# Performance work log

Measured on AMD Instinct MI355X. Metric: run time of the kernel, lower is better.

Reference implementation:

```python
import jax, jax.numpy as jnp
import numpy as np
import math

B, H, S, D = 2, 16, 2048, 128

def setup_inputs() -> dict:
    key = jax.random.key(0)
    kq, kk, kv = jax.random.split(key, 3)
    return {
        "query": jax.random.normal(kq, (B, H, S, D), dtype=jnp.float32),
        "key": jax.random.normal(kk, (B, H, S, D), dtype=jnp.float32),
        "value": jax.random.normal(kv, (B, H, S, D), dtype=jnp.float32),
        "m": 0,  # falsy mask: original's masked_fill was non-in-place (no-op) anyway
    }

def reference(query, key, value, m):
    d = query.shape[-1]
    # scores: [B, H, S, S]
    scores = jnp.einsum("bhqd,bhkd->bhqk", query, key) / math.sqrt(d)
    # NOTE: original torch code's masked_fill is not in-place, so the mask
    # never affects scores; we faithfully skip it (m is falsy here regardless).
    p_attn = jax.nn.softmax(scores, axis=-1)
    p_val = jnp.einsum("bhqk,bhkd->bhqd", p_attn, value)
    return (p_val, p_attn)
```

## Files before the change

kernel.cpp:

```cpp
#include <hip/hip_runtime.h>
#include <hip/hip_bf16.h>
#include <math.h>

#define S_LEN 2048
#define DHEAD 128
#define NH    32
#define BM    128
#define KT    32
#define NKT   (S_LEN / KT)
#define SCALE 0.08838834764831845f
#define CMAX  16.0f

typedef __attribute__((ext_vector_type(4))) float f32x4;
typedef __attribute__((ext_vector_type(8))) _Float16 f16x8;
typedef __attribute__((ext_vector_type(8))) unsigned short u16x8;

static __device__ __forceinline__ f16x8 as_h8(u16x8 x) {
  return __builtin_bit_cast(f16x8, x);
}
static __device__ __forceinline__ unsigned short h16(float x) {
  _Float16 h = (_Float16)x;
  return __builtin_bit_cast(unsigned short, h);
}
static __device__ __forceinline__ void gl16(const void* g, void* l) {
  __builtin_amdgcn_global_load_lds(
      (const __attribute__((address_space(1))) void*)g,
      (__attribute__((address_space(3))) void*)l, 16, 0, 0);
}

__global__ __launch_bounds__(512) void attn_kernel(
    const float* __restrict__ Qg, const float* __restrict__ Kg,
    const float* __restrict__ Vg, float* __restrict__ out) {
  __shared__ __align__(16) float khf32[2][KT * DHEAD];
  __shared__ __align__(16) unsigned short vtr[2][DHEAD * KT];

  const int tid = threadIdx.x;
  const int w  = tid >> 6;
  const int l  = tid & 63;
  const int lr = l & 15;
  const int lg = l >> 4;

  const int d_  = blockIdx.x;
  const int xcd = d_ & 7;
  const int slot = d_ >> 3;
  const int bh = xcd + 8 * (slot >> 4);
  const int qb = slot & 15;

  const size_t head_off = (size_t)bh * S_LEN * DHEAD;
  const float* Qh = Qg + head_off;
  const float* Kh = Kg + head_off;
  const float* Vh = Vg + head_off;
  float* Ov = out + head_off;
  float* Pa = out + (size_t)NH * S_LEN * DHEAD + (size_t)bh * S_LEN * S_LEN;

  const int n0 = w * 128 + l;
  const int r0 = n0 >> 5, gc0 = (n0 & 31) ^ (r0 & 7);
  const int n1 = n0 + 64;
  const int r1 = n1 >> 5, gc1 = (n1 & 31) ^ (r1 & 7);
  const int gk0 = r0 * 128 + gc0 * 4;
  const int gk1 = r1 * 128 + gc1 * 4;
  float* lds_k0a = &khf32[0][(w * 128) * 4];
  float* lds_k0b = &khf32[0][(w * 128 + 64) * 4];
  float* lds_k1a = &khf32[1][(w * 128) * 4];
  float* lds_k1b = &khf32[1][(w * 128 + 64) * 4];

  auto issue_k = [&](int t, int b) {
    const float* src = Kh + (size_t)t * KT * DHEAD;
    gl16(src + gk0, b ? lds_k1a : lds_k0a);
    gl16(src + gk1, b ? lds_k1b : lds_k0b);
  };

  const int vi0 = tid, vi1 = 512 + tid;
  const int vkv0 = (vi0 >> 2) & 31, vd40 = (vi0 & 3) | ((vi0 >> 7) << 2);
  const int vkv1 = (vi1 >> 2) & 31, vd41 = (vi1 & 3) | ((vi1 >> 7) << 2);
  float4 vx0, vx1;
  auto load_v = [&](int t) {
    const float4* sv = (const float4*)(Vh + (size_t)t * KT * DHEAD);
    vx0 = sv[vkv0 * 32 + vd40];
    vx1 = sv[vkv1 * 32 + vd41];
  };
  auto write_v = [&](int b) {
    unsigned short* dst = vtr[b];
    float f0[4] = {vx0.x, vx0.y, vx0.z, vx0.w};
    float f1[4] = {vx1.x, vx1.y, vx1.z, vx1.w};
#pragma unroll
    for (int j = 0; j < 4; ++j) {
      int da = vd40 * 4 + j, db = vd41 * 4 + j;
      dst[da * 32 + (vkv0 ^ (((da >> 1) & 3) << 3))] = h16(f0[j]);
      dst[db * 32 + (vkv1 ^ (((db >> 1) & 3) << 3))] = h16(f1[j]);
    }
  };

  auto ldk = [&](int b, int row, int cc) -> f16x8 {
    const int m = row & 7;
    const float* base = b ? &khf32[1][row * 128] : &khf32[0][row * 128];
    f32x4 a = *(const f32x4*)&base[(cc ^ m) << 2];
    f32x4 c = *(const f32x4*)&base[((cc + 1) ^ m) << 2];
    f16x8 r;
    r[0] = (_Float16)a[0]; r[1] = (_Float16)a[1];
    r[2] = (_Float16)a[2]; r[3] = (_Float16)a[3];
    r[4] = (_Float16)c[0]; r[5] = (_Float16)c[1];
    r[6] = (_Float16)c[2]; r[7] = (_Float16)c[3];
    return r;
  };

  issue_k(0, 0);
  const int qrow = qb * BM + w * 16 + lr;
  const float* qptr = Qh + (size_t)qrow * DHEAD;
  f16x8 qh[4];
#pragma unroll
  for (int kc = 0; kc < 4; ++kc) {
    const float4* qp4 = (const float4*)(qptr + kc * 32 + lg * 8);
    float4 a = qp4[0], b = qp4[1];
    float xs[8] = {a.x, a.y, a.z, a.w, b.x, b.y, b.z, b.w};
#pragma unroll
    for (int i = 0; i < 8; ++i) qh[kc][i] = (_Float16)(xs[i] * SCALE);
  }

  const f32x4 zero4 = {0.f, 0.f, 0.f, 0.f};

  float esum = 0.f;
  for (int t = 0; t < NKT; ++t) {
    const int b = t & 1;
    asm volatile("s_waitcnt vmcnt(0)" ::: "memory");
    __syncthreads();
    if (t + 1 < NKT) issue_k(t + 1, b ^ 1);

    f32x4 sacc0 = zero4, sacc1 = zero4;
    __builtin_amdgcn_s_setprio(1);
#pragma unroll
    for (int kc = 0; kc < 4; ++kc) {
      const int cc = kc * 8 + lg * 2;
      f16x8 ka = ldk(b, lr, cc);
      f16x8 kb = ldk(b, lr + 16, cc);
      sacc0 = __builtin_amdgcn_mfma_f32_16x16x32_f16(ka, qh[kc], sacc0, 0, 0, 0);
      sacc1 = __builtin_amdgcn_mfma_f32_16x16x32_f16(kb, qh[kc], sacc1, 0, 0, 0);
    }
    __builtin_amdgcn_s_setprio(0);
#pragma unroll
    for (int r = 0; r < 4; ++r)
      esum += __expf(sacc0[r] - CMAX) + __expf(sacc1[r] - CMAX);
  }
  issue_k(0, 0);
  load_v(0);
  esum += __shfl_xor(esum, 16);
  esum += __shfl_xor(esum, 32);
  const float off_ = CMAX + logf(esum);

  f32x4 oacc[8];
#pragma unroll
  for (int dt = 0; dt < 8; ++dt) oacc[dt] = zero4;

  float* Prow = Pa + (size_t)(qb * BM + w * 16 + lr) * S_LEN;

  for (int t = 0; t < NKT; ++t) {
    const int b = t & 1;
    write_v(b);
    asm volatile("s_waitcnt vmcnt(0)" ::: "memory");
    __syncthreads();
    if (t + 1 < NKT) {
      issue_k(t + 1, b ^ 1);
      load_v(t + 1);
    }

    f32x4 sacc0 = zero4, sacc1 = zero4;
    __builtin_amdgcn_s_setprio(1);
#pragma unroll
    for (int kc = 0; kc < 4; ++kc) {
      const int cc = kc * 8 + lg * 2;
      f16x8 ka = ldk(b, lr, cc);
      f16x8 kb = ldk(b, lr + 16, cc);
      sacc0 = __builtin_amdgcn_mfma_f32_16x16x32_f16(ka, qh[kc], sacc0, 0, 0, 0);
      sacc1 = __builtin_amdgcn_mfma_f32_16x16x32_f16(kb, qh[kc], sacc1, 0, 0, 0);
    }
    __builtin_amdgcn_s_setprio(0);

    f32x4 pv0, pv1;
#pragma unroll
    for (int r = 0; r < 4; ++r) {
      pv0[r] = __expf(sacc0[r] - off_);
      pv1[r] = __expf(sacc1[r] - off_);
    }
    *(f32x4*)&Prow[t * KT + lg * 4] = pv0;
    *(f32x4*)&Prow[t * KT + 16 + lg * 4] = pv1;

    u16x8 pf;
    {
      unsigned pk[4];
#pragma unroll
      for (int r = 0; r < 4; ++r)
        pk[r] = __builtin_bit_cast(unsigned,
                  __builtin_amdgcn_cvt_pkrtz(pv0[r], pv1[r]));
      const int la = ((lg & 1) * 2) * 16 + lr;
      const int lb = la + 16;
      const bool hi = (lg & 2) != 0;
#pragma unroll
      for (int r = 0; r < 4; ++r) {
        unsigned ta = (unsigned)__shfl((int)pk[r], la, 64);
        unsigned tb = (unsigned)__shfl((int)pk[r], lb, 64);
        pf[r]     = (unsigned short)(hi ? (ta >> 16) : (ta & 0xffffu));
        pf[r + 4] = (unsigned short)(hi ? (tb >> 16) : (tb & 0xffffu));
      }
    }

    __builtin_amdgcn_s_setprio(1);
#pragma unroll
    for (int dt = 0; dt < 8; ++dt) {
      const int row = dt * 16 + lr;
      const unsigned short* vsrc = vtr[b];
      u16x8 vf = *(const u16x8*)&vsrc[row * 32 +
                                      ((lg * 8) ^ (((row >> 1) & 3) << 3))];
      oacc[dt] = __builtin_amdgcn_mfma_f32_16x16x32_f16(
          as_h8(pf), as_h8(vf), oacc[dt], 0, 0, 0);
    }
    __builtin_amdgcn_s_setprio(0);
  }

#pragma unroll
  for (int dt = 0; dt < 8; ++dt) {
#pragma unroll
    for (int r = 0; r < 4; ++r) {
      const int qloc = w * 16 + lg * 4 + r;
      Ov[(size_t)(qb * BM + qloc) * DHEAD + dt * 16 + lr] = oacc[dt][r];
    }
  }
}

extern "C" void kernel_launch(void* const* d_in, const int* in_sizes, int n_in,
                              void* d_out, int out_size, void* d_ws,
                              size_t ws_size, hipStream_t stream) {
  const float* Q = (const float*)d_in[0];
  const float* K = (const float*)d_in[1];
  const float* V = (const float*)d_in[2];
  float* out = (float*)d_out;
  (void)in_sizes; (void)n_in; (void)out_size; (void)d_ws; (void)ws_size;
  dim3 grid(NH * (S_LEN / BM));
  attn_kernel<<<grid, 512, 0, stream>>>(Q, K, V, out);
}
```

Before: 296.4 us.

## Stage K through registers as fp16 in LDS instead of async fp32 LDS loads

Replaces the direct global-to-LDS fp32 K loads with register-staged loads that convert K to fp16 once and write it to a swizzled fp16 LDS tile. Each tile is then read with one 16-byte LDS load per fragment instead of two fp32 loads plus per-use conversion. LDS use drops by half, and launch bounds now request 4 blocks of 512 threads to raise occupancy. The barrier now waits only on lgkmcnt, and global loads for the next tile overlap compute, at the cost of extra registers holding the prefetched K.

```diff
diff --git a/kernel.cpp b/kernel.cpp
--- a/kernel.cpp
+++ b/kernel.cpp
@@ -13,6 +13,7 @@
 
 typedef __attribute__((ext_vector_type(4))) float f32x4;
 typedef __attribute__((ext_vector_type(8))) _Float16 f16x8;
+typedef __attribute__((ext_vector_type(4))) unsigned short u16x4;
 typedef __attribute__((ext_vector_type(8))) unsigned short u16x8;
 
 static __device__ __forceinline__ f16x8 as_h8(u16x8 x) {
@@ -22,16 +23,19 @@
   _Float16 h = (_Float16)x;
   return __builtin_bit_cast(unsigned short, h);
 }
-static __device__ __forceinline__ void gl16(const void* g, void* l) {
-  __builtin_amdgcn_global_load_lds(
-      (const __attribute__((address_space(1))) void*)g,
-      (__attribute__((address_space(3))) void*)l, 16, 0, 0);
-}
-
-__global__ __launch_bounds__(512) void attn_kernel(
+
+#define BAR()                                                   \
+  do {                                                          \
+    __builtin_amdgcn_sched_barrier(0);                          \
+    asm volatile("s_waitcnt lgkmcnt(0)" ::: "memory");          \
+    __builtin_amdgcn_s_barrier();                               \
+    __builtin_amdgcn_sched_barrier(0);                          \
+  } while (0)
+
+__global__ __launch_bounds__(512, 4) void attn_kernel(
     const float* __restrict__ Qg, const float* __restrict__ Kg,
     const float* __restrict__ Vg, float* __restrict__ out) {
-  __shared__ __align__(16) float khf32[2][KT * DHEAD];
+  __shared__ __align__(16) unsigned short khf[2][KT * DHEAD];
   __shared__ __align__(16) unsigned short vtr[2][DHEAD * KT];
 
   const int tid = threadIdx.x;
@@ -53,58 +57,51 @@
   float* Ov = out + head_off;
   float* Pa = out + (size_t)NH * S_LEN * DHEAD + (size_t)bh * S_LEN * S_LEN;
 
-  const int n0 = w * 128 + l;
-  const int r0 = n0 >> 5, gc0 = (n0 & 31) ^ (r0 & 7);
-  const int n1 = n0 + 64;
-  const int r1 = n1 >> 5, gc1 = (n1 & 31) ^ (r1 & 7);
-  const int gk0 = r0 * 128 + gc0 * 4;
-  const int gk1 = r1 * 128 + gc1 * 4;
-  float* lds_k0a = &khf32[0][(w * 128) * 4];
-  float* lds_k0b = &khf32[0][(w * 128 + 64) * 4];
-  float* lds_k1a = &khf32[1][(w * 128) * 4];
-  float* lds_k1b = &khf32[1][(w * 128 + 64) * 4];
-
-  auto issue_k = [&](int t, int b) {
-    const float* src = Kh + (size_t)t * KT * DHEAD;
-    gl16(src + gk0, b ? lds_k1a : lds_k0a);
-    gl16(src + gk1, b ? lds_k1b : lds_k0b);
-  };
-
-  const int vi0 = tid, vi1 = 512 + tid;
-  const int vkv0 = (vi0 >> 2) & 31, vd40 = (vi0 & 3) | ((vi0 >> 7) << 2);
-  const int vkv1 = (vi1 >> 2) & 31, vd41 = (vi1 & 3) | ((vi1 >> 7) << 2);
-  float4 vx0, vx1;
+  const int ki0 = tid, ki1 = 512 + tid;
+  const int kkv0 = ki0 >> 5, kd40 = ki0 & 31;
+  const int kkv1 = ki1 >> 5, kd41 = ki1 & 31;
+  const int vkv0 = (ki0 >> 2) & 31, vd40 = (ki0 & 3) | ((ki0 >> 7) << 2);
+  const int vkv1 = (ki1 >> 2) & 31, vd41 = (ki1 & 3) | ((ki1 >> 7) << 2);
+
+  float4 kxr0, kxr1, vx0, vx1;
+
+  auto load_k = [&](int t) {
+    const float4* s = (const float4*)(Kh + (size_t)t * KT * DHEAD);
+    kxr0 = s[ki0];
+    kxr1 = s[ki1];
+  };
   auto load_v = [&](int t) {
-    const float4* sv = (const float4*)(Vh + (size_t)t * KT * DHEAD);
-    vx0 = sv[vkv0 * 32 + vd40];
-    vx1 = sv[vkv1 * 32 + vd41];
+    const float4* s = (const float4*)(Vh + (size_t)t * KT * DHEAD);
+    vx0 = s[vkv0 * 32 + vd40];
+    vx1 = s[vkv1 * 32 + vd41];
+  };
+  auto wk1 = [&](unsigned short* dst, int kv, int d4, float4 v) {
+    u16x4 hv;
+    hv[0] = h16(v.x); hv[1] = h16(v.y); hv[2] = h16(v.z); hv[3] = h16(v.w);
+    *(u16x4*)&dst[kv * 128 + (((d4 >> 1) ^ (kv & 7)) << 3) + ((d4 & 1) << 2)] = hv;
+  };
+  auto write_k = [&](int b) {
+    wk1(khf[b], kkv0, kd40, kxr0);
+    wk1(khf[b], kkv1, kd41, kxr1);
+  };
+  auto wv1 = [&](unsigned short* dst, int kv, int d4, float4 v) {
+    float f[4] = {v.x, v.y, v.z, v.w};
+#pragma unroll
+    for (int j = 0; j < 4; ++j) {
+      int d = d4 * 4 + j;
+      dst[d * 32 + (kv ^ (((d >> 1) & 3) << 3))] = h16(f[j]);
+    }
   };
   auto write_v = [&](int b) {
-    unsigned short* dst = vtr[b];
-    float f0[4] = {vx0.x, vx0.y, vx0.z, vx0.w};
-    float f1[4] = {vx1.x, vx1.y, vx1.z, vx1.w};
-#pragma unroll
-    for (int j = 0; j < 4; ++j) {
-      int da = vd40 * 4 + j, db = vd41 * 4 + j;
-      dst[da * 32 + (vkv0 ^ (((da >> 1) & 3) << 3))] = h16(f0[j]);
-      dst[db * 32 + (vkv1 ^ (((db >> 1) & 3) << 3))] = h16(f1[j]);
-    }
-  };
-
-  auto ldk = [&](int b, int row, int cc) -> f16x8 {
-    const int m = row & 7;
-    const float* base = b ? &khf32[1][row * 128] : &khf32[0][row * 128];
-    f32x4 a = *(const f32x4*)&base[(cc ^ m) << 2];
-    f32x4 c = *(const f32x4*)&base[((cc + 1) ^ m) << 2];
-    f16x8 r;
-    r[0] = (_Float16)a[0]; r[1] = (_Float16)a[1];
-    r[2] = (_Float16)a[2]; r[3] = (_Float16)a[3];
-    r[4] = (_Float16)c[0]; r[5] = (_Float16)c[1];
-    r[6] = (_Float16)c[2]; r[7] = (_Float16)c[3];
-    return r;
-  };
-
-  issue_k(0, 0);
+    wv1(vtr[b], vkv0, vd40, vx0);
+    wv1(vtr[b], vkv1, vd41, vx1);
+  };
+  auto ldk = [&](int b, int row, int kc) -> f16x8 {
+    const unsigned short* base = khf[b] + row * 128;
+    return as_h8(*(const u16x8*)&base[(((kc * 4 + lg) ^ (row & 7)) << 3)]);
+  };
+
+  load_k(0);
   const int qrow = qb * BM + w * 16 + lr;
   const float* qptr = Qh + (size_t)qrow * DHEAD;
   f16x8 qh[4];
@@ -122,17 +119,21 @@
   float esum = 0.f;
   for (int t = 0; t < NKT; ++t) {
     const int b = t & 1;
-    asm volatile("s_waitcnt vmcnt(0)" ::: "memory");
-    __syncthreads();
-    if (t + 1 < NKT) issue_k(t + 1, b ^ 1);
+    write_k(b);
+    BAR();
+    if (t + 1 < NKT) {
+      load_k(t + 1);
+    } else {
+      load_k(0);
+      load_v(0);
+    }
 
     f32x4 sacc0 = zero4, sacc1 = zero4;
     __builtin_amdgcn_s_setprio(1);
 #pragma unroll
     for (int kc = 0; kc < 4; ++kc) {
-      const int cc = kc * 8 + lg * 2;
-      f16x8 ka = ldk(b, lr, cc);
-      f16x8 kb = ldk(b, lr + 16, cc);
+      f16x8 ka = ldk(b, lr, kc);
+      f16x8 kb = ldk(b, lr + 16, kc);
       sacc0 = __builtin_amdgcn_mfma_f32_16x16x32_f16(ka, qh[kc], sacc0, 0, 0, 0);
       sacc1 = __builtin_amdgcn_mfma_f32_16x16x32_f16(kb, qh[kc], sacc1, 0, 0, 0);
     }
@@ -141,8 +142,6 @@
     for (int r = 0; r < 4; ++r)
       esum += __expf(sacc0[r] - CMAX) + __expf(sacc1[r] - CMAX);
   }
-  issue_k(0, 0);
-  load_v(0);
   esum += __shfl_xor(esum, 16);
   esum += __shfl_xor(esum, 32);
   const float off_ = CMAX + logf(esum);
@@ -155,11 +154,11 @@
 
   for (int t = 0; t < NKT; ++t) {
     const int b = t & 1;
+    write_k(b);
     write_v(b);
-    asm volatile("s_waitcnt vmcnt(0)" ::: "memory");
-    __syncthreads();
+    BAR();
     if (t + 1 < NKT) {
-      issue_k(t + 1, b ^ 1);
+      load_k(t + 1);
       load_v(t + 1);
     }
 
@@ -167,9 +166,8 @@
     __builtin_amdgcn_s_setprio(1);
 #pragma unroll
     for (int kc = 0; kc < 4; ++kc) {
-      const int cc = kc * 8 + lg * 2;
-      f16x8 ka = ldk(b, lr, cc);
-      f16x8 kb = ldk(b, lr + 16, cc);
+      f16x8 ka = ldk(b, lr, kc);
+      f16x8 kb = ldk(b, lr + 16, kc);
       sacc0 = __builtin_amdgcn_mfma_f32_16x16x32_f16(ka, qh[kc], sacc0, 0, 0, 0);
       sacc1 = __builtin_amdgcn_mfma_f32_16x16x32_f16(kb, qh[kc], sacc1, 0, 0, 0);
     }
```

New measurement: 301.1 us. Within noise of the previous version (+1.6%).

## Deepen K/V prefetch to distance two with partial vmcnt waits

Applied to the files above, without the earlier changes.

Grows the K LDS ring from two to four buffers and prefetches K two tiles ahead in both passes. V tiles are now double-buffered in registers (two sets) and also loaded two tiles ahead. Full vmcnt(0)+__syncthreads is replaced by sched-barrier-fenced partial vmcnt waits plus an lgkmcnt wait and s_barrier, aiming to hide global load latency behind MFMA work. It also sets a min-waves-per-EU launch bound; the trade-off is more LDS per block (80KB), which may limit occupancy, and vmcnt bookkeeping that must stay correct when interleaved with P stores.

```diff
diff --git a/kernel.cpp b/kernel.cpp
--- a/kernel.cpp
+++ b/kernel.cpp
@@ -28,10 +28,24 @@
       (__attribute__((address_space(3))) void*)l, 16, 0, 0);
 }
 
-__global__ __launch_bounds__(512) void attn_kernel(
+#define BAR()                                                   \
+  do {                                                          \
+    __builtin_amdgcn_sched_barrier(0);                          \
+    asm volatile("s_waitcnt lgkmcnt(0)" ::: "memory");          \
+    __builtin_amdgcn_s_barrier();                               \
+    __builtin_amdgcn_sched_barrier(0);                          \
+  } while (0)
+#define WAITV(n)                                                \
+  do {                                                          \
+    __builtin_amdgcn_sched_barrier(0);                          \
+    asm volatile("s_waitcnt vmcnt(" #n ")" ::: "memory");       \
+    __builtin_amdgcn_sched_barrier(0);                          \
+  } while (0)
+
+__global__ __launch_bounds__(512, 4) void attn_kernel(
     const float* __restrict__ Qg, const float* __restrict__ Kg,
     const float* __restrict__ Vg, float* __restrict__ out) {
-  __shared__ __align__(16) float khf32[2][KT * DHEAD];
+  __shared__ __align__(16) float kbuf[4][KT * DHEAD];
   __shared__ __align__(16) unsigned short vtr[2][DHEAD * KT];
 
   const int tid = threadIdx.x;
@@ -59,41 +73,15 @@
   const int r1 = n1 >> 5, gc1 = (n1 & 31) ^ (r1 & 7);
   const int gk0 = r0 * 128 + gc0 * 4;
   const int gk1 = r1 * 128 + gc1 * 4;
-  float* lds_k0a = &khf32[0][(w * 128) * 4];
-  float* lds_k0b = &khf32[0][(w * 128 + 64) * 4];
-  float* lds_k1a = &khf32[1][(w * 128) * 4];
-  float* lds_k1b = &khf32[1][(w * 128 + 64) * 4];
-
   auto issue_k = [&](int t, int b) {
     const float* src = Kh + (size_t)t * KT * DHEAD;
-    gl16(src + gk0, b ? lds_k1a : lds_k0a);
-    gl16(src + gk1, b ? lds_k1b : lds_k0b);
+    float* base = &kbuf[b][w * 512];
+    gl16(src + gk0, base);
+    gl16(src + gk1, base + 256);
   };
-
-  const int vi0 = tid, vi1 = 512 + tid;
-  const int vkv0 = (vi0 >> 2) & 31, vd40 = (vi0 & 3) | ((vi0 >> 7) << 2);
-  const int vkv1 = (vi1 >> 2) & 31, vd41 = (vi1 & 3) | ((vi1 >> 7) << 2);
-  float4 vx0, vx1;
-  auto load_v = [&](int t) {
-    const float4* sv = (const float4*)(Vh + (size_t)t * KT * DHEAD);
-    vx0 = sv[vkv0 * 32 + vd40];
-    vx1 = sv[vkv1 * 32 + vd41];
-  };
-  auto write_v = [&](int b) {
-    unsigned short* dst = vtr[b];
-    float f0[4] = {vx0.x, vx0.y, vx0.z, vx0.w};
-    float f1[4] = {vx1.x, vx1.y, vx1.z, vx1.w};
-#pragma unroll
-    for (int j = 0; j < 4; ++j) {
-      int da = vd40 * 4 + j, db = vd41 * 4 + j;
-      dst[da * 32 + (vkv0 ^ (((da >> 1) & 3) << 3))] = h16(f0[j]);
-      dst[db * 32 + (vkv1 ^ (((db >> 1) & 3) << 3))] = h16(f1[j]);
-    }
-  };
-
   auto ldk = [&](int b, int row, int cc) -> f16x8 {
     const int m = row & 7;
-    const float* base = b ? &khf32[1][row * 128] : &khf32[0][row * 128];
+    const float* base = &kbuf[b][row * 128];
     f32x4 a = *(const f32x4*)&base[(cc ^ m) << 2];
     f32x4 c = *(const f32x4*)&base[((cc + 1) ^ m) << 2];
     f16x8 r;
@@ -104,7 +92,21 @@
     return r;
   };
 
+  const int vi0 = tid, vi1 = 512 + tid;
+  const int vkv0 = (vi0 >> 2) & 31, vd40 = (vi0 & 3) | ((vi0 >> 7) << 2);
+  const int vkv1 = (vi1 >> 2) & 31, vd41 = (vi1 & 3) | ((vi1 >> 7) << 2);
+  float4 vxa0, vxa1, vxb0, vxb1;
+  auto wv1 = [&](unsigned short* dst, int kv, int d4, float4 v) {
+    float f[4] = {v.x, v.y, v.z, v.w};
+#pragma unroll
+    for (int j = 0; j < 4; ++j) {
+      int d = d4 * 4 + j;
+      dst[d * 32 + (kv ^ (((d >> 1) & 3) << 3))] = h16(f[j]);
+    }
+  };
+
   issue_k(0, 0);
+  issue_k(1, 1);
   const int qrow = qb * BM + w * 16 + lr;
   const float* qptr = Qh + (size_t)qrow * DHEAD;
   f16x8 qh[4];
@@ -121,10 +123,10 @@
 
   float esum = 0.f;
   for (int t = 0; t < NKT; ++t) {
-    const int b = t & 1;
-    asm volatile("s_waitcnt vmcnt(0)" ::: "memory");
-    __syncthreads();
-    if (t + 1 < NKT) issue_k(t + 1, b ^ 1);
+    const int b = t & 3;
+    if (t < NKT - 1) WAITV(2); else WAITV(0);
+    if (t + 2 < NKT) issue_k(t + 2, (t + 2) & 3);
+    BAR();
 
     f32x4 sacc0 = zero4, sacc1 = zero4;
     __builtin_amdgcn_s_setprio(1);
@@ -141,8 +143,17 @@
     for (int r = 0; r < 4; ++r)
       esum += __expf(sacc0[r] - CMAX) + __expf(sacc1[r] - CMAX);
   }
-  issue_k(0, 0);
-  load_v(0);
+
+  {
+    const float4* sv0 = (const float4*)Vh;
+    vxa0 = sv0[vkv0 * 32 + vd40];
+    vxa1 = sv0[vkv1 * 32 + vd41];
+    issue_k(0, 0);
+    const float4* sv1 = (const float4*)(Vh + (size_t)KT * DHEAD);
+    vxb0 = sv1[vkv0 * 32 + vd40];
+    vxb1 = sv1[vkv1 * 32 + vd41];
+    issue_k(1, 1);
+  }
   esum += __shfl_xor(esum, 16);
   esum += __shfl_xor(esum, 32);
   const float off_ = CMAX + logf(esum);
@@ -154,14 +165,28 @@
   float* Prow = Pa + (size_t)(qb * BM + w * 16 + lr) * S_LEN;
 
   for (int t = 0; t < NKT; ++t) {
-    const int b = t & 1;
-    write_v(b);
-    asm volatile("s_waitcnt vmcnt(0)" ::: "memory");
-    __syncthreads();
-    if (t + 1 < NKT) {
-      issue_k(t + 1, b ^ 1);
-      load_v(t + 1);
-    }
+    const int b = t & 3;
+    if ((t & 1) == 0) {
+      wv1(vtr[0], vkv0, vd40, vxa0);
+      wv1(vtr[0], vkv1, vd41, vxa1);
+      WAITV(4);
+      if (t + 2 < NKT) {
+        const float4* sv = (const float4*)(Vh + (size_t)(t + 2) * KT * DHEAD);
+        vxa0 = sv[vkv0 * 32 + vd40];
+        vxa1 = sv[vkv1 * 32 + vd41];
+      }
+    } else {
+      wv1(vtr[1], vkv0, vd40, vxb0);
+      wv1(vtr[1], vkv1, vd41, vxb1);
+      WAITV(4);
+      if (t + 2 < NKT) {
+        const float4* sv = (const float4*)(Vh + (size_t)(t + 2) * KT * DHEAD);
+        vxb0 = sv[vkv0 * 32 + vd40];
+        vxb1 = sv[vkv1 * 32 + vd41];
+      }
+    }
+    if (t + 2 < NKT) issue_k(t + 2, (t + 2) & 3);
+    BAR();
 
     f32x4 sacc0 = zero4, sacc1 = zero4;
     __builtin_amdgcn_s_setprio(1);
@@ -204,10 +229,10 @@
     }
 
     __builtin_amdgcn_s_setprio(1);
+    const unsigned short* vsrc = vtr[t & 1];
 #pragma unroll
     for (int dt = 0; dt < 8; ++dt) {
       const int row = dt * 16 + lr;
-      const unsigned short* vsrc = vtr[b];
       u16x8 vf = *(const u16x8*)&vsrc[row * 32 +
                                       ((lg * 8) ^ (((row >> 1) & 3) << 3))];
       oacc[dt] = __builtin_amdgcn_mfma_f32_16x16x32_f16(
```

Result: slower. 333.8 us (+12.6%).
